# Kernel tuning notes

Measured on AMD Instinct MI355X. Metric: run time of the kernel, lower is better.

The kernel has to match this reference:

```python
import jax, jax.numpy as jnp
import numpy as np

B, S, DIM, H = 8, 1024, 1024, 16
D = DIM // H  # d_head = 64


def setup_inputs() -> dict:
    key = jax.random.key(0)
    ks = jax.random.split(key, 7)
    scale = 1.0 / np.sqrt(D)  # nn.Linear default init range ~ U(-1/sqrt(in), 1/sqrt(in))
    x = jax.random.normal(ks[0], (B, S, DIM), dtype=jnp.float32)
    Wq = jax.random.uniform(ks[1], (H, D, D), jnp.float32, -scale, scale)
    Wk = jax.random.uniform(ks[2], (H, D, D), jnp.float32, -scale, scale)
    Wv = jax.random.uniform(ks[3], (H, D, D), jnp.float32, -scale, scale)
    bq = jax.random.uniform(ks[4], (H, D), jnp.float32, -scale, scale)
    bk = jax.random.uniform(ks[5], (H, D), jnp.float32, -scale, scale)
    bv = jax.random.uniform(ks[6], (H, D), jnp.float32, -scale, scale)
    return {"x": x, "Wq": Wq, "Wk": Wk, "Wv": Wv, "bq": bq, "bk": bk, "bv": bv}


def reference(x, Wq, Wk, Wv, bq, bk, bv):
    # x: [B,S,DIM] -> split heads: [B,S,H,D] (matches per-head column slicing)
    xh = x.reshape(x.shape[0], x.shape[1], H, D)
    # per-head linear: y = x @ W.T + b  (nn.Linear convention: weight [out,in])
    q = jnp.einsum('bshd,hed->bshe', xh, Wq) + bq  # [B,S,H,D]
    k = jnp.einsum('bshd,hed->bshe', xh, Wk) + bk
    v = jnp.einsum('bshd,hed->bshe', xh, Wv) + bv
    scores = jnp.einsum('bqhd,bkhd->bhqk', q, k) / jnp.sqrt(jnp.float32(D))
    attn = jax.nn.softmax(scores, axis=-1)  # [B,H,S,S]
    out = jnp.einsum('bhqk,bkhd->bqhd', attn, v)  # [B,S,H,D]
    # hstack over heads == merge last two dims back to DIM
    return out.reshape(x.shape[0], x.shape[1], H * D)
```

## Files before the change

### kernel.cpp

```cpp
#include <hip/hip_runtime.h>
#include <hip/hip_bf16.h>

#define BB 8
#define SS 1024
#define HH 16
#define DD 64
#define DIMM 1024
#define NUNITS (BB * HH)
#define UNIT_ELEMS (SS * DD)

typedef __attribute__((ext_vector_type(8))) short short8;
typedef __attribute__((ext_vector_type(4))) float f32x4;
typedef __attribute__((ext_vector_type(16))) float f32x16;
typedef __attribute__((ext_vector_type(2))) unsigned u32x2;
typedef __attribute__((ext_vector_type(4))) unsigned u32x4;

#if __has_builtin(__builtin_amdgcn_exp2f)
#define EXP2F(x) __builtin_amdgcn_exp2f(x)
#else
#define EXP2F(x) exp2f(x)
#endif
#if __has_builtin(__builtin_amdgcn_rcpf)
#define RCPF(x) __builtin_amdgcn_rcpf(x)
#else
#define RCPF(x) (1.0f / (x))
#endif

__device__ inline short f2b(float f) {
    unsigned u = __float_as_uint(f);
    u = (u + 0x7FFFu + ((u >> 16) & 1u)) >> 16;
    return (short)u;
}

__device__ __forceinline__ unsigned cvtpk_bf16(float lo, float hi) {
    unsigned r;
    asm("v_cvt_pk_bf16_f32 %0, %1, %2" : "=v"(r) : "v"(lo), "v"(hi));
    return r;
}

__device__ __forceinline__ void gll16(const void* g, void* l) {
    __builtin_amdgcn_global_load_lds(
        (const __attribute__((address_space(1))) void*)g,
        (__attribute__((address_space(3))) void*)l,
        16, 0, 0);
}

__global__ __launch_bounds__(256) void qkv_proj(
    const float* __restrict__ x, const float* __restrict__ Wq,
    const float* __restrict__ Wk, const float* __restrict__ Wv,
    const float* __restrict__ bqp, const float* __restrict__ bkp,
    const float* __restrict__ bvp,
    short* __restrict__ Qo, short* __restrict__ Ko, short* __restrict__ Vto,
    int unit0)
{
    __shared__ alignas(16) short wsm[3][64][72];
    __shared__ alignas(16) short xs[64][72];
    __shared__ alignas(16) short tr[64][72];

    const int t = threadIdx.x;
    const int bid = blockIdx.x;
    const int stg = bid & 3;
    const int ul = bid >> 2;
    const int unit = unit0 + ul;
    const int h = unit & 15;
    const int b = unit >> 4;

    for (int m = 0; m < 3; ++m) {
        const float* src = ((m == 0) ? Wq : (m == 1) ? Wk : Wv) + h * DD * DD;
        for (int i = 0; i < 4; ++i) {
            int g = t + i * 256;
            int e = g >> 4, c = (g & 15) * 4;
            float4 wv = *reinterpret_cast<const float4*>(src + e * DD + c);
            short4 sv; sv.x = f2b(wv.x); sv.y = f2b(wv.y); sv.z = f2b(wv.z); sv.w = f2b(wv.w);
            *reinterpret_cast<short4*>(&wsm[m][e][c]) = sv;
        }
    }

    const int lane = t & 63, w = t >> 6;
    const int l15 = lane & 15, quad = lane >> 4;

    for (int st2 = 0; st2 < 4; ++st2) {
        const int s0 = (stg * 4 + st2) * 64;
        if (st2) __syncthreads();
        for (int i = 0; i < 4; ++i) {
            int g = t + i * 256;
            int r = g >> 4, c = (g & 15) * 4;
            float4 xv = *reinterpret_cast<const float4*>(
                x + ((size_t)(b * SS + s0 + r)) * DIMM + h * DD + c);
            short4 sv; sv.x = f2b(xv.x); sv.y = f2b(xv.y); sv.z = f2b(xv.z); sv.w = f2b(xv.w);
            *reinterpret_cast<short4*>(&xs[r][c]) = sv;
        }
        __syncthreads();

        short8 a0 = *reinterpret_cast<const short8*>(&xs[w * 16 + l15][quad * 8]);
        short8 a1 = *reinterpret_cast<const short8*>(&xs[w * 16 + l15][32 + quad * 8]);

        f32x4 acc[12];
        for (int m = 0; m < 3; ++m)
            for (int et = 0; et < 4; ++et) {
                short8 w0 = *reinterpret_cast<const short8*>(&wsm[m][et * 16 + l15][quad * 8]);
                short8 w1 = *reinterpret_cast<const short8*>(&wsm[m][et * 16 + l15][32 + quad * 8]);
                f32x4 a = {0.f, 0.f, 0.f, 0.f};
                a = __builtin_amdgcn_mfma_f32_16x16x32_bf16(a0, w0, a, 0, 0, 0);
                a = __builtin_amdgcn_mfma_f32_16x16x32_bf16(a1, w1, a, 0, 0, 0);
                acc[m * 4 + et] = a;
            }

        for (int m = 0; m < 3; ++m) {
            if (m) __syncthreads();
            const float* bp = (m == 0) ? bqp : (m == 1) ? bkp : bvp;
            const float scale = (m == 0) ? 0.125f : 1.0f;
            for (int et = 0; et < 4; ++et) {
                float bias = bp[h * DD + et * 16 + l15];
                int e = et * 16 + l15;
                for (int r = 0; r < 4; ++r) {
                    float v = (acc[m * 4 + et][r] + bias) * scale;
                    int srow = w * 16 + quad * 4 + r;
                    if (m == 2) tr[e][srow] = f2b(v);
                    else        tr[srow][e] = f2b(v);
                }
            }
            __syncthreads();
            for (int i = 0; i < 2; ++i) {
                int g = t + i * 256;
                int row = g >> 3, col = (g & 7) * 8;
                short8 val = *reinterpret_cast<const short8*>(&tr[row][col]);
                if (m == 0)
                    *reinterpret_cast<short8*>(Qo + ((size_t)ul * SS + s0 + row) * DD + col) = val;
                else if (m == 1)
                    *reinterpret_cast<short8*>(Ko + ((size_t)ul * SS + s0 + row) * DD + col) = val;
                else
                    *reinterpret_cast<short8*>(Vto + ((size_t)ul * DD + row) * SS + s0 + col) = val;
            }
        }
    }
}

__global__ __launch_bounds__(256, 4) void attn(
    const short* __restrict__ Q, const short* __restrict__ K,
    const short* __restrict__ Vt, float* __restrict__ out, int unit0, int nu)
{
    __shared__ alignas(16) short ksm[2][64][64];
    __shared__ alignas(16) short vsm[2][64][64];
    __shared__ float lsm[4][32];

    const int t = threadIdx.x;
    const int bid = blockIdx.x;
    int ul, qt;
    if (nu == NUNITS) {
        int xslot = bid & 7;
        int j = bid >> 3;
        ul = xslot * 16 + (j & 15);
        qt = j >> 4;
    } else {
        ul = bid >> 3;
        qt = bid & 7;
    }
    const int unit = unit0 + ul;
    const int h = unit & 15;
    const int b = unit >> 4;
    const int q0 = qt * 128;
    const int lane = t & 63, w = t >> 6;
    const int r5 = lane & 31;
    const int hi = lane >> 5;
    const int l7 = lane & 7;
    const int hl4 = (hi ^ l7) << 4;

    short8 qb[4];
    {
        const short* qp = Q + ((size_t)ul * SS + q0 + w * 32 + r5) * DD + hi * 8;
#pragma unroll
        for (int ds = 0; ds < 4; ++ds)
            qb[ds] = *reinterpret_cast<const short8*>(qp + ds * 16);
    }

    const int lrow = lane >> 3, lch = (lane & 7) ^ lrow;
    const short* kg = K + (size_t)ul * UNIT_ELEMS + (size_t)(w * 8 + lrow) * DD + lch * 8;
    const short* vg = Vt + ((size_t)ul * DD + w * 8 + lrow) * SS + lch * 8;

    const char* kread0 = (const char*)&ksm[0][0][0] + r5 * 128;
    const char* vread0 = (const char*)&vsm[0][0][0] + r5 * 128;

    f32x16 o0, o1;
#pragma unroll
    for (int i = 0; i < 16; ++i) { o0[i] = 0.f; o1[i] = 0.f; }
    float lsum = 0.f;

    const float L2E = 1.44269504f;
    const float MBIAS = 11.5415603f;

    {
        short* lk = &ksm[0][w * 8][0];
        short* lv = &vsm[0][w * 8][0];
        gll16(kg, lk); gll16(kg + 32 * DD, lk + 32 * 64);
        gll16(vg, lv); gll16(vg + 32 * SS, lv + 32 * 64);
        kg += 64 * DD; vg += 64;
    }

    for (int kt = 0; kt < 16; ++kt) {
        const int cur = kt & 1;
        __syncthreads();

        if (kt < 15) {
            const int nxt = cur ^ 1;
            short* lk = &ksm[nxt][w * 8][0];
            short* lv = &vsm[nxt][w * 8][0];
            gll16(kg, lk); gll16(kg + 32 * DD, lk + 32 * 64);
            gll16(vg, lv); gll16(vg + 32 * SS, lv + 32 * 64);
            kg += 64 * DD; vg += 64;
        }

        const char* kb_ = kread0 + cur * 8192;
        const char* vb_ = vread0 + cur * 8192;

        f32x16 c0, c1;
#pragma unroll
        for (int i = 0; i < 16; ++i) { c0[i] = 0.f; c1[i] = 0.f; }

        __builtin_amdgcn_s_setprio(1);
#pragma unroll
        for (int ds = 0; ds < 4; ++ds) {
            short8 ka = *reinterpret_cast<const short8*>(kb_ + ((ds << 5) ^ hl4));
            short8 kb = *reinterpret_cast<const short8*>(kb_ + 4096 + ((ds << 5) ^ hl4));
            c0 = __builtin_amdgcn_mfma_f32_32x32x16_bf16(ka, qb[ds], c0, 0, 0, 0);
            c1 = __builtin_amdgcn_mfma_f32_32x32x16_bf16(kb, qb[ds], c1, 0, 0, 0);
        }
        __builtin_amdgcn_s_setprio(0);

#pragma unroll
        for (int n = 0; n < 2; ++n) {
            f32x16 c = n ? c1 : c0;
            float p[16];
#pragma unroll
            for (int r = 0; r < 16; ++r)
                p[r] = EXP2F(fmaf(c[r], L2E, -MBIAS));
            lsum += ((((p[0] + p[1]) + (p[2] + p[3])) + ((p[4] + p[5]) + (p[6] + p[7])))
                   + (((p[8] + p[9]) + (p[10] + p[11])) + ((p[12] + p[13]) + (p[14] + p[15]))));

#pragma unroll
            for (int bb2 = 0; bb2 < 2; ++bb2) {
                unsigned u0 = cvtpk_bf16(p[8 * bb2 + 0], p[8 * bb2 + 1]);
                unsigned u1 = cvtpk_bf16(p[8 * bb2 + 2], p[8 * bb2 + 3]);
                unsigned v0 = cvtpk_bf16(p[8 * bb2 + 4], p[8 * bb2 + 5]);
                unsigned v1 = cvtpk_bf16(p[8 * bb2 + 6], p[8 * bb2 + 7]);
                unsigned w0, w1c, w2, w3;
#if __has_builtin(__builtin_amdgcn_permlane32_swap)
                u32x2 r0 = __builtin_amdgcn_permlane32_swap(u0, v0, false, false);
                u32x2 r1 = __builtin_amdgcn_permlane32_swap(u1, v1, false, false);
                w0 = r0[0]; w2 = r0[1]; w1c = r1[0]; w3 = r1[1];
#else
                unsigned u0s = __shfl_xor(u0, 32), v0s = __shfl_xor(v0, 32);
                unsigned u1s = __shfl_xor(u1, 32), v1s = __shfl_xor(v1, 32);
                w0 = hi ? v0s : u0;  w2 = hi ? v0 : u0s;
                w1c = hi ? v1s : u1; w3 = hi ? v1 : u1s;
#endif
                u32x4 aw; aw[0] = w0; aw[1] = w1c; aw[2] = w2; aw[3] = w3;
                short8 af = __builtin_bit_cast(short8, aw);

                const int ks = n * 2 + bb2;
                short8 va = *reinterpret_cast<const short8*>(vb_ + ((ks << 5) ^ hl4));
                short8 vb2 = *reinterpret_cast<const short8*>(vb_ + 4096 + ((ks << 5) ^ hl4));
                __builtin_amdgcn_s_setprio(1);
                o0 = __builtin_amdgcn_mfma_f32_32x32x16_bf16(af, va, o0, 0, 0, 0);
                o1 = __builtin_amdgcn_mfma_f32_32x32x16_bf16(af, vb2, o1, 0, 0, 0);
                __builtin_amdgcn_s_setprio(0);
            }
        }
    }

    float lt = lsum + __shfl_xor(lsum, 32);
    if (lane < 32) lsm[w][lane] = lt;

#pragma unroll
    for (int reg = 0; reg < 16; ++reg) {
        const int row = (reg & 3) + 8 * (reg >> 2) + 4 * hi;
        float rin = RCPF(lsm[w][row]);
        float* op = out + ((size_t)(b * SS + q0 + w * 32 + row)) * DIMM + h * DD + r5;
        op[0]  = o0[reg] * rin;
        op[32] = o1[reg] * rin;
    }
}

extern "C" void kernel_launch(void* const* d_in, const int* in_sizes, int n_in,
                              void* d_out, int out_size, void* d_ws, size_t ws_size,
                              hipStream_t stream) {
    const float* x   = (const float*)d_in[0];
    const float* Wq  = (const float*)d_in[1];
    const float* Wk  = (const float*)d_in[2];
    const float* Wv  = (const float*)d_in[3];
    const float* bqp = (const float*)d_in[4];
    const float* bkp = (const float*)d_in[5];
    const float* bvp = (const float*)d_in[6];
    float* out = (float*)d_out;

    const size_t unit_bytes = 3ULL * UNIT_ELEMS * sizeof(short);
    int U = (int)(ws_size / unit_bytes);
    if (U < 1) U = 1;
    if (U > NUNITS) U = NUNITS;

    short* Qw  = (short*)d_ws;
    short* Kw  = Qw + (size_t)U * UNIT_ELEMS;
    short* Vtw = Kw + (size_t)U * UNIT_ELEMS;

    for (int u0 = 0; u0 < NUNITS; u0 += U) {
        int nu = NUNITS - u0 < U ? NUNITS - u0 : U;
        qkv_proj<<<dim3(nu * 4), dim3(256), 0, stream>>>(
            x, Wq, Wk, Wv, bqp, bkp, bvp, Qw, Kw, Vtw, u0);
        attn<<<dim3(nu * 8), dim3(256), 0, stream>>>(Qw, Kw, Vtw, out, u0, nu);
    }
}
```

Before: 149.2 us.

## Restructure QKV projection with 32x32 MFMA tiles and single-barrier output staging

The QKV projection kernel switches from 16x16x32 MFMA tiles to 32x32x16 tiles, with each wave computing a 32x32 output block for Q, K and V. It stages all three results in separate LDS buffers so they are written out after one barrier instead of three. The Q scale is folded into the weights and bias, and bf16 packing is done two values at a time. In attention, the first QK MFMA now takes a zero vector as its accumulator instead of explicitly zeroed registers, and the softmax/PV code is moved into a macro. The extra LDS buffers raise shared memory use, which may lower occupancy.

```diff
diff --git a/kernel.cpp b/kernel.cpp
--- a/kernel.cpp
+++ b/kernel.cpp
@@ -31,11 +31,28 @@
     u = (u + 0x7FFFu + ((u >> 16) & 1u)) >> 16;
     return (short)u;
 }
+__device__ inline unsigned pk2(float lo, float hi) {
+    unsigned a = __float_as_uint(lo), b = __float_as_uint(hi);
+    a = (a + 0x7FFFu + ((a >> 16) & 1u)) >> 16;
+    b = (b + 0x7FFFu + ((b >> 16) & 1u)) & 0xFFFF0000u;
+    return a | b;
+}
 
 __device__ __forceinline__ unsigned cvtpk_bf16(float lo, float hi) {
     unsigned r;
     asm("v_cvt_pk_bf16_f32 %0, %1, %2" : "=v"(r) : "v"(lo), "v"(hi));
     return r;
+}
+
+__device__ __forceinline__ u32x2 plswap(unsigned a, unsigned b, int hi) {
+#if __has_builtin(__builtin_amdgcn_permlane32_swap)
+    u32x2 r = __builtin_amdgcn_permlane32_swap(a, b, false, false);
+    return r;
+#else
+    unsigned as = __shfl_xor(a, 32), bs = __shfl_xor(b, 32);
+    u32x2 r; r[0] = hi ? bs : a; r[1] = hi ? b : as;
+    return r;
+#endif
 }
 
 __device__ __forceinline__ void gll16(const void* g, void* l) {
@@ -55,7 +72,9 @@
 {
     __shared__ alignas(16) short wsm[3][64][72];
     __shared__ alignas(16) short xs[64][72];
-    __shared__ alignas(16) short tr[64][72];
+    __shared__ alignas(16) short trq[64][72];
+    __shared__ alignas(16) short trk[64][72];
+    __shared__ alignas(16) short trv[64][72];
 
     const int t = threadIdx.x;
     const int bid = blockIdx.x;
@@ -65,73 +84,87 @@
     const int h = unit & 15;
     const int b = unit >> 4;
 
+    const int lane = t & 63, w = t >> 6;
+    const int l31 = lane & 31, hi = lane >> 5;
+    const int shalf = w & 1, ehalf = w >> 1;
+    const int ecol = ehalf * 32 + l31;
+
     for (int m = 0; m < 3; ++m) {
         const float* src = ((m == 0) ? Wq : (m == 1) ? Wk : Wv) + h * DD * DD;
+        const float ws = (m == 0) ? 0.125f : 1.0f;
         for (int i = 0; i < 4; ++i) {
             int g = t + i * 256;
             int e = g >> 4, c = (g & 15) * 4;
-            float4 wv = *reinterpret_cast<const float4*>(src + e * DD + c);
-            short4 sv; sv.x = f2b(wv.x); sv.y = f2b(wv.y); sv.z = f2b(wv.z); sv.w = f2b(wv.w);
-            *reinterpret_cast<short4*>(&wsm[m][e][c]) = sv;
-        }
-    }
-
-    const int lane = t & 63, w = t >> 6;
-    const int l15 = lane & 15, quad = lane >> 4;
-
-    for (int st2 = 0; st2 < 4; ++st2) {
-        const int s0 = (stg * 4 + st2) * 64;
-        if (st2) __syncthreads();
+            float4 wv4 = *reinterpret_cast<const float4*>(src + e * DD + c);
+            u32x2 pk; pk[0] = pk2(wv4.x * ws, wv4.y * ws);
+            pk[1] = pk2(wv4.z * ws, wv4.w * ws);
+            *reinterpret_cast<u32x2*>(&wsm[m][e][c]) = pk;
+        }
+    }
+    const float bq_ = bqp[h * DD + ecol] * 0.125f;
+    const float bk_ = bkp[h * DD + ecol];
+    const float bv_ = bvp[h * DD + ecol];
+
+    f32x16 zv;
+#pragma unroll
+    for (int i = 0; i < 16; ++i) zv[i] = 0.f;
+
+    for (int st = 0; st < 4; ++st) {
+        const int s0 = (stg * 4 + st) * 64;
         for (int i = 0; i < 4; ++i) {
             int g = t + i * 256;
             int r = g >> 4, c = (g & 15) * 4;
             float4 xv = *reinterpret_cast<const float4*>(
                 x + ((size_t)(b * SS + s0 + r)) * DIMM + h * DD + c);
-            short4 sv; sv.x = f2b(xv.x); sv.y = f2b(xv.y); sv.z = f2b(xv.z); sv.w = f2b(xv.w);
-            *reinterpret_cast<short4*>(&xs[r][c]) = sv;
+            u32x2 pk; pk[0] = pk2(xv.x, xv.y); pk[1] = pk2(xv.z, xv.w);
+            *reinterpret_cast<u32x2*>(&xs[r][c]) = pk;
         }
         __syncthreads();
 
-        short8 a0 = *reinterpret_cast<const short8*>(&xs[w * 16 + l15][quad * 8]);
-        short8 a1 = *reinterpret_cast<const short8*>(&xs[w * 16 + l15][32 + quad * 8]);
-
-        f32x4 acc[12];
-        for (int m = 0; m < 3; ++m)
-            for (int et = 0; et < 4; ++et) {
-                short8 w0 = *reinterpret_cast<const short8*>(&wsm[m][et * 16 + l15][quad * 8]);
-                short8 w1 = *reinterpret_cast<const short8*>(&wsm[m][et * 16 + l15][32 + quad * 8]);
-                f32x4 a = {0.f, 0.f, 0.f, 0.f};
-                a = __builtin_amdgcn_mfma_f32_16x16x32_bf16(a0, w0, a, 0, 0, 0);
-                a = __builtin_amdgcn_mfma_f32_16x16x32_bf16(a1, w1, a, 0, 0, 0);
-                acc[m * 4 + et] = a;
+        short8 a[4];
+#pragma unroll
+        for (int ks = 0; ks < 4; ++ks)
+            a[ks] = *reinterpret_cast<const short8*>(&xs[shalf * 32 + l31][ks * 16 + hi * 8]);
+
+        f32x16 cm[3];
+#pragma unroll
+        for (int m = 0; m < 3; ++m) {
+            short8 wb0 = *reinterpret_cast<const short8*>(&wsm[m][ecol][hi * 8]);
+            f32x16 c = __builtin_amdgcn_mfma_f32_32x32x16_bf16(a[0], wb0, zv, 0, 0, 0);
+#pragma unroll
+            for (int ks = 1; ks < 4; ++ks) {
+                short8 wb = *reinterpret_cast<const short8*>(&wsm[m][ecol][ks * 16 + hi * 8]);
+                c = __builtin_amdgcn_mfma_f32_32x32x16_bf16(a[ks], wb, c, 0, 0, 0);
             }
-
-        for (int m = 0; m < 3; ++m) {
-            if (m) __syncthreads();
-            const float* bp = (m == 0) ? bqp : (m == 1) ? bkp : bvp;
-            const float scale = (m == 0) ? 0.125f : 1.0f;
-            for (int et = 0; et < 4; ++et) {
-                float bias = bp[h * DD + et * 16 + l15];
-                int e = et * 16 + l15;
-                for (int r = 0; r < 4; ++r) {
-                    float v = (acc[m * 4 + et][r] + bias) * scale;
-                    int srow = w * 16 + quad * 4 + r;
-                    if (m == 2) tr[e][srow] = f2b(v);
-                    else        tr[srow][e] = f2b(v);
-                }
-            }
-            __syncthreads();
-            for (int i = 0; i < 2; ++i) {
-                int g = t + i * 256;
-                int row = g >> 3, col = (g & 7) * 8;
-                short8 val = *reinterpret_cast<const short8*>(&tr[row][col]);
-                if (m == 0)
-                    *reinterpret_cast<short8*>(Qo + ((size_t)ul * SS + s0 + row) * DD + col) = val;
-                else if (m == 1)
-                    *reinterpret_cast<short8*>(Ko + ((size_t)ul * SS + s0 + row) * DD + col) = val;
-                else
-                    *reinterpret_cast<short8*>(Vto + ((size_t)ul * DD + row) * SS + s0 + col) = val;
-            }
+            cm[m] = c;
+        }
+
+#pragma unroll
+        for (int reg = 0; reg < 16; ++reg) {
+            int srow = shalf * 32 + (reg & 3) + 8 * (reg >> 2) + 4 * hi;
+            trq[srow][ecol] = f2b(cm[0][reg] + bq_);
+            trk[srow][ecol] = f2b(cm[1][reg] + bk_);
+        }
+#pragma unroll
+        for (int rq = 0; rq < 4; ++rq) {
+            int sbase = shalf * 32 + 4 * hi + 8 * rq;
+            u32x2 pk;
+            pk[0] = pk2(cm[2][4 * rq + 0] + bv_, cm[2][4 * rq + 1] + bv_);
+            pk[1] = pk2(cm[2][4 * rq + 2] + bv_, cm[2][4 * rq + 3] + bv_);
+            *reinterpret_cast<u32x2*>(&trv[ecol][sbase]) = pk;
+        }
+        __syncthreads();
+
+#pragma unroll
+        for (int i = 0; i < 2; ++i) {
+            int cidx = t + i * 256;
+            int row = cidx >> 3, col8 = (cidx & 7) * 8;
+            short8 vq = *reinterpret_cast<const short8*>(&trq[row][col8]);
+            short8 vk = *reinterpret_cast<const short8*>(&trk[row][col8]);
+            short8 vv = *reinterpret_cast<const short8*>(&trv[row][col8]);
+            *reinterpret_cast<short8*>(Qo + ((size_t)ul * SS + s0 + row) * DD + col8) = vq;
+            *reinterpret_cast<short8*>(Ko + ((size_t)ul * SS + s0 + row) * DD + col8) = vk;
+            *reinterpret_cast<short8*>(Vto + ((size_t)ul * DD + row) * SS + s0 + col8) = vv;
         }
     }
 }
@@ -181,9 +214,10 @@
     const char* kread0 = (const char*)&ksm[0][0][0] + r5 * 128;
     const char* vread0 = (const char*)&vsm[0][0][0] + r5 * 128;
 
-    f32x16 o0, o1;
-#pragma unroll
-    for (int i = 0; i < 16; ++i) { o0[i] = 0.f; o1[i] = 0.f; }
+    f32x16 zv;
+#pragma unroll
+    for (int i = 0; i < 16; ++i) zv[i] = 0.f;
+    f32x16 o0 = zv, o1 = zv;
     float lsum = 0.f;
 
     const float L2E = 1.44269504f;
@@ -196,6 +230,32 @@
         gll16(vg, lv); gll16(vg + 32 * SS, lv + 32 * 64);
         kg += 64 * DD; vg += 64;
     }
+
+#define SMPV(CV, NOFF) do {                                                      \
+    float p_[16];                                                                \
+    _Pragma("unroll")                                                            \
+    for (int r_ = 0; r_ < 16; ++r_) p_[r_] = EXP2F(fmaf(CV[r_], L2E, -MBIAS));   \
+    lsum += ((((p_[0]+p_[1])+(p_[2]+p_[3]))+((p_[4]+p_[5])+(p_[6]+p_[7])))       \
+           +(((p_[8]+p_[9])+(p_[10]+p_[11]))+((p_[12]+p_[13])+(p_[14]+p_[15])))); \
+    _Pragma("unroll")                                                            \
+    for (int b2_ = 0; b2_ < 2; ++b2_) {                                          \
+        unsigned u0_ = cvtpk_bf16(p_[8*b2_+0], p_[8*b2_+1]);                     \
+        unsigned u1_ = cvtpk_bf16(p_[8*b2_+2], p_[8*b2_+3]);                     \
+        unsigned v0_ = cvtpk_bf16(p_[8*b2_+4], p_[8*b2_+5]);                     \
+        unsigned v1_ = cvtpk_bf16(p_[8*b2_+6], p_[8*b2_+7]);                     \
+        u32x2 r0_ = plswap(u0_, v0_, hi);                                        \
+        u32x2 r1_ = plswap(u1_, v1_, hi);                                        \
+        u32x4 aw_; aw_[0] = r0_[0]; aw_[1] = r1_[0]; aw_[2] = r0_[1]; aw_[3] = r1_[1]; \
+        short8 af_ = __builtin_bit_cast(short8, aw_);                            \
+        const int ks_ = (NOFF) * 2 + b2_;                                        \
+        short8 va_ = *reinterpret_cast<const short8*>(vb_ + ((ks_ << 5) ^ hl4)); \
+        short8 vb2_ = *reinterpret_cast<const short8*>(vb_ + 4096 + ((ks_ << 5) ^ hl4)); \
+        __builtin_amdgcn_s_setprio(1);                                           \
+        o0 = __builtin_amdgcn_mfma_f32_32x32x16_bf16(af_, va_, o0, 0, 0, 0);     \
+        o1 = __builtin_amdgcn_mfma_f32_32x32x16_bf16(af_, vb2_, o1, 0, 0, 0);    \
+        __builtin_amdgcn_s_setprio(0);                                           \
+    }                                                                            \
+} while (0)
 
     for (int kt = 0; kt < 16; ++kt) {
         const int cur = kt & 1;
@@ -214,12 +274,15 @@
         const char* vb_ = vread0 + cur * 8192;
 
         f32x16 c0, c1;
-#pragma unroll
-        for (int i = 0; i < 16; ++i) { c0[i] = 0.f; c1[i] = 0.f; }
-
         __builtin_amdgcn_s_setprio(1);
-#pragma unroll
-        for (int ds = 0; ds < 4; ++ds) {
+        {
+            short8 ka = *reinterpret_cast<const short8*>(kb_ + hl4);
+            short8 kb = *reinterpret_cast<const short8*>(kb_ + 4096 + hl4);
+            c0 = __builtin_amdgcn_mfma_f32_32x32x16_bf16(ka, qb[0], zv, 0, 0, 0);
+            c1 = __builtin_amdgcn_mfma_f32_32x32x16_bf16(kb, qb[0], zv, 0, 0, 0);
+        }
+#pragma unroll
+        for (int ds = 1; ds < 4; ++ds) {
             short8 ka = *reinterpret_cast<const short8*>(kb_ + ((ds << 5) ^ hl4));
             short8 kb = *reinterpret_cast<const short8*>(kb_ + 4096 + ((ds << 5) ^ hl4));
             c0 = __builtin_amdgcn_mfma_f32_32x32x16_bf16(ka, qb[ds], c0, 0, 0, 0);
@@ -227,46 +290,10 @@
         }
         __builtin_amdgcn_s_setprio(0);
 
-#pragma unroll
-        for (int n = 0; n < 2; ++n) {
-            f32x16 c = n ? c1 : c0;
-            float p[16];
-#pragma unroll
-            for (int r = 0; r < 16; ++r)
-                p[r] = EXP2F(fmaf(c[r], L2E, -MBIAS));
-            lsum += ((((p[0] + p[1]) + (p[2] + p[3])) + ((p[4] + p[5]) + (p[6] + p[7])))
-                   + (((p[8] + p[9]) + (p[10] + p[11])) + ((p[12] + p[13]) + (p[14] + p[15]))));
-
-#pragma unroll
-            for (int bb2 = 0; bb2 < 2; ++bb2) {
-                unsigned u0 = cvtpk_bf16(p[8 * bb2 + 0], p[8 * bb2 + 1]);
-                unsigned u1 = cvtpk_bf16(p[8 * bb2 + 2], p[8 * bb2 + 3]);
-                unsigned v0 = cvtpk_bf16(p[8 * bb2 + 4], p[8 * bb2 + 5]);
-                unsigned v1 = cvtpk_bf16(p[8 * bb2 + 6], p[8 * bb2 + 7]);
-                unsigned w0, w1c, w2, w3;
-#if __has_builtin(__builtin_amdgcn_permlane32_swap)
-                u32x2 r0 = __builtin_amdgcn_permlane32_swap(u0, v0, false, false);
-                u32x2 r1 = __builtin_amdgcn_permlane32_swap(u1, v1, false, false);
-                w0 = r0[0]; w2 = r0[1]; w1c = r1[0]; w3 = r1[1];
-#else
-                unsigned u0s = __shfl_xor(u0, 32), v0s = __shfl_xor(v0, 32);
-                unsigned u1s = __shfl_xor(u1, 32), v1s = __shfl_xor(v1, 32);
-                w0 = hi ? v0s : u0;  w2 = hi ? v0 : u0s;
-                w1c = hi ? v1s : u1; w3 = hi ? v1 : u1s;
-#endif
-                u32x4 aw; aw[0] = w0; aw[1] = w1c; aw[2] = w2; aw[3] = w3;
-                short8 af = __builtin_bit_cast(short8, aw);
-
-                const int ks = n * 2 + bb2;
-                short8 va = *reinterpret_cast<const short8*>(vb_ + ((ks << 5) ^ hl4));
-                short8 vb2 = *reinterpret_cast<const short8*>(vb_ + 4096 + ((ks << 5) ^ hl4));
-                __builtin_amdgcn_s_setprio(1);
-                o0 = __builtin_amdgcn_mfma_f32_32x32x16_bf16(af, va, o0, 0, 0, 0);
-                o1 = __builtin_amdgcn_mfma_f32_32x32x16_bf16(af, vb2, o1, 0, 0, 0);
-                __builtin_amdgcn_s_setprio(0);
-            }
-        }
-    }
+        SMPV(c0, 0);
+        SMPV(c1, 1);
+    }
+#undef SMPV
 
     float lt = lsum + __shfl_xor(lsum, 32);
     if (lane < 32) lsm[w][lane] = lt;
```

Result: faster. 144.0 us, median of 2 (-3.5%).
